# Kernel tuning notes

Hardware: AMD Instinct MI355X
Metric: run time of the kernel (lower is better)

Reference implementation:

```python
import jax, jax.numpy as jnp
import numpy as np

OUT_SIZE = 7      # roi_layer out_size
SAMPLE_NUM = 2    # roi_layer sample_num
STRIDES = (4, 8, 16, 32)
IMG = 1024.0


def _roi_align(feat_nchw, rois, out, scale, sn):
    """mmdet RoIAlign (aligned=False), vectorized over all rois.

    feat_nchw: [B, C, H, W]; rois: [N, 5] = (batch_idx, x1, y1, x2, y2).
    Returns [N, C, out, out].
    """
    feat = jnp.transpose(feat_nchw, (0, 2, 3, 1))  # [B, H, W, C]
    B, H, W, C = feat.shape
    N = rois.shape[0]
    b = rois[:, 0].astype(jnp.int32)
    x1 = rois[:, 1] * scale
    y1 = rois[:, 2] * scale
    x2 = rois[:, 3] * scale
    y2 = rois[:, 4] * scale
    roi_w = jnp.maximum(x2 - x1, 1.0)
    roi_h = jnp.maximum(y2 - y1, 1.0)
    # sample-point offsets within the roi, in bin units: [out*sn]
    grid = (jnp.arange(out, dtype=jnp.float32)[:, None]
            + (jnp.arange(sn, dtype=jnp.float32)[None, :] + 0.5) / sn).reshape(-1)
    ys = y1[:, None] + grid[None, :] * (roi_h / out)[:, None]  # [N, S]
    xs = x1[:, None] + grid[None, :] * (roi_w / out)[:, None]  # [N, S]

    def interp1(coord, size):
        valid = ((coord > -1.0) & (coord < size)).astype(coord.dtype)
        c = jnp.clip(coord, 0.0, size - 1.0)
        lo = jnp.floor(c).astype(jnp.int32)
        hi = jnp.minimum(lo + 1, size - 1)
        w_hi = c - lo.astype(coord.dtype)
        w_lo = 1.0 - w_hi
        # zero-out out-of-image samples via the weights
        return lo, hi, w_lo * valid, w_hi * valid

    y_lo, y_hi, wy_lo, wy_hi = interp1(ys, H)
    x_lo, x_hi, wx_lo, wx_hi = interp1(xs, W)

    def gather(yi, xi):
        # [N, S, S, C]
        return feat[b[:, None, None], yi[:, :, None], xi[:, None, :]]

    val = (gather(y_lo, x_lo) * (wy_lo[:, :, None] * wx_lo[:, None, :])[..., None]
           + gather(y_lo, x_hi) * (wy_lo[:, :, None] * wx_hi[:, None, :])[..., None]
           + gather(y_hi, x_lo) * (wy_hi[:, :, None] * wx_lo[:, None, :])[..., None]
           + gather(y_hi, x_hi) * (wy_hi[:, :, None] * wx_hi[:, None, :])[..., None])
    # average the sn x sn samples inside each bin
    val = val.reshape(N, out, sn, out, sn, C).mean(axis=(2, 4))  # [N, out, out, C]
    return jnp.transpose(val, (0, 3, 1, 2))  # [N, C, out, out]


def setup_inputs() -> dict:
    key = jax.random.key(0)
    ks = jax.random.split(key, 8)
    feats = {}
    for i, hw in enumerate([256, 128, 64, 32]):
        feats[f"feat{i}"] = jax.random.normal(ks[i], (1, 256, hw, hw), dtype=jnp.float32)
    N = 1000
    u = jax.random.uniform(ks[4], (N, 4), dtype=jnp.float32)
    x1 = u[:, 0] * (IMG - 64.0)
    y1 = u[:, 1] * (IMG - 64.0)
    w = 16.0 + u[:, 2] * 480.0
    h = 16.0 + u[:, 3] * 480.0
    x2 = jnp.minimum(x1 + w, IMG - 1.0)
    y2 = jnp.minimum(y1 + h, IMG - 1.0)
    bidx = jnp.zeros((N,), dtype=jnp.float32)
    rois = jnp.stack([bidx, x1, y1, x2, y2], axis=1)
    feats["rois"] = rois
    return feats


def reference(feat0, feat1, feat2, feat3, rois):
    feats = (feat0, feat1, feat2, feat3)
    # PASingleRoIExtractor multi-level path: RoIAlign every roi on every level,
    # then elementwise max across levels.
    out = _roi_align(feats[0], rois, OUT_SIZE, 1.0 / STRIDES[0], SAMPLE_NUM)
    for lvl in range(1, len(feats)):
        out = jnp.maximum(out, _roi_align(feats[lvl], rois, OUT_SIZE,
                                          1.0 / STRIDES[lvl], SAMPLE_NUM))
    return out
```

## Files before the change

kernel.cpp:

```cpp
#include <hip/hip_runtime.h>


#define NCH 256
#define NBIN 49

typedef _Float16 half2v __attribute__((ext_vector_type(2)));

#if defined(__has_builtin)
#if __has_builtin(__builtin_amdgcn_fdot2)
#define HAVE_FDOT2 1
#endif
#if __has_builtin(__builtin_amdgcn_cvt_pkrtz)
#define HAVE_PKRTZ 1
#endif
#endif

__device__ __constant__ int    d_H[4]      = {256, 128, 64, 32};
__device__ __constant__ float  d_scale[4]  = {0.25f, 0.125f, 0.0625f, 0.03125f};
__device__ __constant__ unsigned d_off4b[4] = {0u, 33554432u, 41943040u, 44040192u};
__device__ __constant__ size_t d_offu[4]   = {0, 16777216, 20971520, 22020096};
__device__ __constant__ int    d_P[4]      = {65536, 16384, 4096, 1024};
__device__ __constant__ int    d_t2s[4]    = {0, 2048, 2560, 2688};
__device__ __constant__ int    d_psh[4]    = {9, 7, 5, 3};

__device__ __forceinline__ int pack_h2(float a, float b) {
#ifdef HAVE_PKRTZ
    return __builtin_bit_cast(int, __builtin_amdgcn_cvt_pkrtz(a, b));
#else
    half2v h;
    h.x = (_Float16)a;
    h.y = (_Float16)b;
    return __builtin_bit_cast(int, h);
#endif
}
__device__ __forceinline__ half2v bc_h2(int x) { return __builtin_bit_cast(half2v, x); }
__device__ __forceinline__ half2v bc_h2u(unsigned x) { return __builtin_bit_cast(half2v, x); }

#ifdef HAVE_FDOT2
#define ACC2(uLLc, uLHc, w2, k0)                                                                       \
    acc[k0] = __builtin_amdgcn_fdot2(bc_h2u(__builtin_amdgcn_perm((uLHc), (uLLc), 0x05040100u)), (w2), \
                                     acc[k0], false);                                                  \
    acc[k0 + 1] = __builtin_amdgcn_fdot2(                                                              \
        bc_h2u(__builtin_amdgcn_perm((uLHc), (uLLc), 0x07060302u)), (w2), acc[k0 + 1], false)
#else
#define ACC2(uLLc, uLHc, w2, k0)                                       \
    do {                                                               \
        half2v a_ = bc_h2u(uLLc), b_ = bc_h2u(uLHc);                   \
        float w0_ = (float)(w2).x, w1_ = (float)(w2).y;                \
        acc[k0]     = fmaf((float)a_.x, w0_, acc[k0]);                 \
        acc[k0]     = fmaf((float)b_.x, w1_, acc[k0]);                 \
        acc[k0 + 1] = fmaf((float)a_.y, w0_, acc[k0 + 1]);             \
        acc[k0 + 1] = fmaf((float)b_.y, w1_, acc[k0 + 1]);             \
    } while (0)
#endif

__device__ __forceinline__ void math4(float* acc, const uint4* L, int4 ye, int4 xe) {
    half2v wx = bc_h2(xe.z);
    half2v wlo = bc_h2(ye.z) * wx;
    half2v whi = bc_h2(ye.w) * wx;
    ACC2(L[0].x, L[1].x, wlo, 0);
    ACC2(L[0].y, L[1].y, wlo, 2);
    ACC2(L[0].z, L[1].z, wlo, 4);
    ACC2(L[0].w, L[1].w, wlo, 6);
    ACC2(L[2].x, L[3].x, whi, 0);
    ACC2(L[2].y, L[3].y, whi, 2);
    ACC2(L[2].z, L[3].z, whi, 4);
    ACC2(L[2].w, L[3].w, whi, 6);
}

__device__ __forceinline__ uint4 ldws(const char* __restrict__ wsb, unsigned off) {
    return *(const uint4*)(wsb + off);
}

__global__ __launch_bounds__(256) void transpose_flat(
    const float* __restrict__ f0, const float* __restrict__ f1, const float* __restrict__ f2,
    const float* __restrict__ f3, unsigned short* __restrict__ out) {
    const int b = blockIdx.x;
    const int lvl = (b >= d_t2s[1]) + (b >= d_t2s[2]) + (b >= d_t2s[3]);
    const int rem = b - d_t2s[lvl];
    const int sh = d_psh[lvl];
    const int pb = rem & ((1 << sh) - 1);
    const int cgi = rem >> sh;
    const int P = d_P[lvl];
    const float* in = (lvl == 0) ? f0 : (lvl == 1) ? f1 : (lvl == 2) ? f2 : f3;

    const int tid = threadIdx.x;
    const int o8 = tid & 7;
    const int g = tid >> 3;
    const int p0 = pb * 128 + g * 4;
    const int c0 = cgi * 64 + o8 * 8;

    const float* src = in + (size_t)c0 * P + p0;
    float vv[32];
#pragma unroll
    for (int r = 0; r < 8; ++r)
        *(float4*)&vv[4 * r] = *(const float4*)(src + (size_t)r * P);

    unsigned short* o = out + d_offu[lvl] + (size_t)p0 * NCH + c0;
#pragma unroll
    for (int j = 0; j < 4; ++j) {
        uint4 d;
        d.x = (unsigned)pack_h2(vv[0 * 4 + j], vv[1 * 4 + j]);
        d.y = (unsigned)pack_h2(vv[2 * 4 + j], vv[3 * 4 + j]);
        d.z = (unsigned)pack_h2(vv[4 * 4 + j], vv[5 * 4 + j]);
        d.w = (unsigned)pack_h2(vv[6 * 4 + j], vv[7 * 4 + j]);
        *(uint4*)(o + (size_t)j * NCH) = d;
    }
}

__global__ __launch_bounds__(256, 4) void roi_main4b(const uint4* __restrict__ ws,
                                                     const float* __restrict__ rois,
                                                     float* __restrict__ out) {
    __shared__ float smem[64 * NBIN];
    __shared__ int4 tbl[4][2][14];

    const int n = blockIdx.x >> 2;
    const int quarter = blockIdx.x & 3;
    const int tid = threadIdx.x;
    const float* r = rois + (size_t)n * 5;

    if (tid < 112) {
        int lvl = tid / 28;
        int e = tid % 28;
        int axis = e / 14;
        int s = e % 14;
        int H = d_H[lvl];
        float sc = d_scale[lvl];
        float a = (axis ? r[1] : r[2]) * sc;
        float b2 = (axis ? r[3] : r[4]) * sc;
        float binsz = fmaxf(b2 - a, 1.0f) * (1.0f / 7.0f);
        float g = (float)(s >> 1) + 0.25f + 0.5f * (float)(s & 1);
        float coord = a + g * binsz;
        float valid = (coord > -1.0f && coord < (float)H) ? 1.0f : 0.0f;
        float c = fminf(fmaxf(coord, 0.0f), (float)H - 1.0f);
        int lo = (int)floorf(c);
        int hi = min(lo + 1, H - 1);
        float whi = (c - (float)lo) * valid;
        float wlo = (1.0f - (c - (float)lo)) * valid;
        int mult = axis ? 512 : H * 512;
        int4 t;
        t.x = lo * mult;
        t.y = hi * mult;
        if (axis) {
            t.z = pack_h2(wlo, whi);
            t.w = 0;
        } else {
            t.z = pack_h2(wlo, wlo);
            t.w = pack_h2(whi, whi);
        }
        tbl[lvl][axis][s] = t;
    }
    __syncthreads();

    const int p = tid & 7;
    const int h = tid >> 3;
    const int octet = quarter * 8 + p;
    const char* __restrict__ wsb = (const char*)ws;

    unsigned lvlbase[4];
#pragma unroll
    for (int l = 0; l < 4; ++l) lvlbase[l] = d_off4b[l] + (unsigned)octet * 16u;

#pragma unroll
    for (int pass = 0; pass < 2; ++pass) {
        const int b = h + pass * 32;
        if (b < NBIN) {
            int by = b / 7;
            int bx = b - by * 7;
            float m[8];
#pragma unroll
            for (int k = 0; k < 8; ++k) m[k] = -3.402823e38f;
#pragma unroll
            for (int lvl = 0; lvl < 4; ++lvl) {
                const unsigned base = lvlbase[lvl];
                int4 ye0 = tbl[lvl][0][2 * by];
                int4 ye1 = tbl[lvl][0][2 * by + 1];
                int4 xe0 = tbl[lvl][1][2 * bx];
                int4 xe1 = tbl[lvl][1][2 * bx + 1];
                uint4 L[16];
                L[0]  = ldws(wsb, base + (unsigned)(ye0.x + xe0.x));
                L[1]  = ldws(wsb, base + (unsigned)(ye0.x + xe0.y));
                L[2]  = ldws(wsb, base + (unsigned)(ye0.y + xe0.x));
                L[3]  = ldws(wsb, base + (unsigned)(ye0.y + xe0.y));
                L[4]  = ldws(wsb, base + (unsigned)(ye0.x + xe1.x));
                L[5]  = ldws(wsb, base + (unsigned)(ye0.x + xe1.y));
                L[6]  = ldws(wsb, base + (unsigned)(ye0.y + xe1.x));
                L[7]  = ldws(wsb, base + (unsigned)(ye0.y + xe1.y));
                L[8]  = ldws(wsb, base + (unsigned)(ye1.x + xe0.x));
                L[9]  = ldws(wsb, base + (unsigned)(ye1.x + xe0.y));
                L[10] = ldws(wsb, base + (unsigned)(ye1.y + xe0.x));
                L[11] = ldws(wsb, base + (unsigned)(ye1.y + xe0.y));
                L[12] = ldws(wsb, base + (unsigned)(ye1.x + xe1.x));
                L[13] = ldws(wsb, base + (unsigned)(ye1.x + xe1.y));
                L[14] = ldws(wsb, base + (unsigned)(ye1.y + xe1.x));
                L[15] = ldws(wsb, base + (unsigned)(ye1.y + xe1.y));
                float acc[8];
#pragma unroll
                for (int k = 0; k < 8; ++k) acc[k] = 0.0f;
                math4(acc, &L[0], ye0, xe0);
                math4(acc, &L[4], ye0, xe1);
                math4(acc, &L[8], ye1, xe0);
                math4(acc, &L[12], ye1, xe1);
#pragma unroll
                for (int k = 0; k < 8; ++k) m[k] = fmaxf(m[k], acc[k] * 0.25f);
            }
#pragma unroll
            for (int k = 0; k < 8; ++k) smem[(p * 8 + k) * NBIN + b] = m[k];
        }
    }
    __syncthreads();

    float4* o4 = (float4*)(out + (size_t)n * (NCH * NBIN) + (size_t)quarter * (64 * NBIN));
    const float4* s4 = (const float4*)smem;
    for (int i = tid; i < 64 * NBIN / 4; i += 256) o4[i] = s4[i];
}

__device__ __forceinline__ int4 make_entry_f(float coord, int size, int mult) {
    float valid = (coord > -1.0f && coord < (float)size) ? 1.0f : 0.0f;
    float c = fminf(fmaxf(coord, 0.0f), (float)size - 1.0f);
    int lo = (int)floorf(c);
    int hi = min(lo + 1, size - 1);
    float whi = (c - (float)lo) * valid;
    float wlo = (1.0f - (c - (float)lo)) * valid;
    int4 r;
    r.x = lo * mult;
    r.y = hi * mult;
    r.z = __float_as_int(wlo);
    r.w = __float_as_int(whi);
    return r;
}

__global__ __launch_bounds__(256) void roi_direct(
    const float* __restrict__ f0, const float* __restrict__ f1, const float* __restrict__ f2,
    const float* __restrict__ f3, const float* __restrict__ rois, float* __restrict__ out) {
    const int n = blockIdx.x;
    const int c = threadIdx.x;
    const float* feats[4] = {f0, f1, f2, f3};
    const float* r = rois + (size_t)n * 5;
    for (int b = 0; b < NBIN; ++b) {
        int by = b / 7;
        int bx = b - by * 7;
        float m = -3.402823e38f;
#pragma unroll
        for (int lvl = 0; lvl < 4; ++lvl) {
            int H = d_H[lvl];
            float sc = d_scale[lvl];
            float x1 = r[1] * sc, y1 = r[2] * sc, x2 = r[3] * sc, y2 = r[4] * sc;
            float bw = fmaxf(x2 - x1, 1.0f) * (1.0f / 7.0f);
            float bh = fmaxf(y2 - y1, 1.0f) * (1.0f / 7.0f);
            const float* f = feats[lvl] + (size_t)c * H * H;
            float acc = 0.0f;
#pragma unroll
            for (int sy = 0; sy < 2; ++sy) {
#pragma unroll
                for (int sx = 0; sx < 2; ++sx) {
                    float yc = y1 + ((float)by + 0.25f + 0.5f * sy) * bh;
                    float xc = x1 + ((float)bx + 0.25f + 0.5f * sx) * bw;
                    int4 ey = make_entry_f(yc, H, H);
                    int4 ex = make_entry_f(xc, H, 1);
                    float wyl = __int_as_float(ey.z), wyh = __int_as_float(ey.w);
                    float wxl = __int_as_float(ex.z), wxh = __int_as_float(ex.w);
                    acc += f[ey.x + ex.x] * wyl * wxl + f[ey.x + ex.y] * wyl * wxh +
                           f[ey.y + ex.x] * wyh * wxl + f[ey.y + ex.y] * wyh * wxh;
                }
            }
            m = fmaxf(m, acc * 0.25f);
        }
        out[((size_t)n * NCH + c) * NBIN + b] = m;
    }
}

extern "C" void kernel_launch(void* const* d_in, const int* in_sizes, int n_in, void* d_out,
                              int out_size, void* d_ws, size_t ws_size, hipStream_t stream) {
    const float* f0 = (const float*)d_in[0];
    const float* f1 = (const float*)d_in[1];
    const float* f2 = (const float*)d_in[2];
    const float* f3 = (const float*)d_in[3];
    const float* rois = (const float*)d_in[4];
    const int nrois = in_sizes[4] / 5;
    float* out = (float*)d_out;

    const size_t need = 44564480;
    if (ws_size < need) {
        roi_direct<<<nrois, 256, 0, stream>>>(f0, f1, f2, f3, rois, out);
        return;
    }
    unsigned short* wsp = (unsigned short*)d_ws;
    transpose_flat<<<2720, 256, 0, stream>>>(f0, f1, f2, f3, wsp);
    roi_main4b<<<4 * nrois, 256, 0, stream>>>((const uint4*)d_ws, rois, out);
}
```

Baseline: 204.7 us.

## Double-buffer per-level gathers with sched barriers to overlap loads and math

Restructures the per-bin level loop into a two-buffer software pipeline. The next level's 16 gather loads are issued before the current level's interpolation math runs, and sched_barrier fences keep the compiler from reordering them. Launch bounds drop from 4 to 2 blocks per CU to make room for the extra registers the doubled load buffers need. The aim is to hide gather latency inside each wave, at the cost of fewer resident waves to hide latency across waves.

```diff
diff --git a/kernel.cpp b/kernel.cpp
--- a/kernel.cpp
+++ b/kernel.cpp
@@ -72,6 +72,39 @@
     return *(const uint4*)(wsb + off);
 }
 
+__device__ __forceinline__ void issue16(uint4* L, const char* __restrict__ wsb, unsigned base,
+                                        int4 ye0, int4 ye1, int4 xe0, int4 xe1) {
+    L[0]  = ldws(wsb, base + (unsigned)(ye0.x + xe0.x));
+    L[1]  = ldws(wsb, base + (unsigned)(ye0.x + xe0.y));
+    L[2]  = ldws(wsb, base + (unsigned)(ye0.y + xe0.x));
+    L[3]  = ldws(wsb, base + (unsigned)(ye0.y + xe0.y));
+    L[4]  = ldws(wsb, base + (unsigned)(ye0.x + xe1.x));
+    L[5]  = ldws(wsb, base + (unsigned)(ye0.x + xe1.y));
+    L[6]  = ldws(wsb, base + (unsigned)(ye0.y + xe1.x));
+    L[7]  = ldws(wsb, base + (unsigned)(ye0.y + xe1.y));
+    L[8]  = ldws(wsb, base + (unsigned)(ye1.x + xe0.x));
+    L[9]  = ldws(wsb, base + (unsigned)(ye1.x + xe0.y));
+    L[10] = ldws(wsb, base + (unsigned)(ye1.y + xe0.x));
+    L[11] = ldws(wsb, base + (unsigned)(ye1.y + xe0.y));
+    L[12] = ldws(wsb, base + (unsigned)(ye1.x + xe1.x));
+    L[13] = ldws(wsb, base + (unsigned)(ye1.x + xe1.y));
+    L[14] = ldws(wsb, base + (unsigned)(ye1.y + xe1.x));
+    L[15] = ldws(wsb, base + (unsigned)(ye1.y + xe1.y));
+}
+
+__device__ __forceinline__ void math_stage(float* m, const uint4* L, int4 ye0, int4 ye1,
+                                           int4 xe0, int4 xe1) {
+    float acc[8];
+#pragma unroll
+    for (int k = 0; k < 8; ++k) acc[k] = 0.0f;
+    math4(acc, &L[0], ye0, xe0);
+    math4(acc, &L[4], ye0, xe1);
+    math4(acc, &L[8], ye1, xe0);
+    math4(acc, &L[12], ye1, xe1);
+#pragma unroll
+    for (int k = 0; k < 8; ++k) m[k] = fmaxf(m[k], acc[k] * 0.25f);
+}
+
 __global__ __launch_bounds__(256) void transpose_flat(
     const float* __restrict__ f0, const float* __restrict__ f1, const float* __restrict__ f2,
     const float* __restrict__ f3, unsigned short* __restrict__ out) {
@@ -108,7 +141,7 @@
     }
 }
 
-__global__ __launch_bounds__(256, 4) void roi_main4b(const uint4* __restrict__ ws,
+__global__ __launch_bounds__(256, 2) void roi_main4b(const uint4* __restrict__ ws,
                                                      const float* __restrict__ rois,
                                                      float* __restrict__ out) {
     __shared__ float smem[64 * NBIN];
@@ -161,6 +194,15 @@
 #pragma unroll
     for (int l = 0; l < 4; ++l) lvlbase[l] = d_off4b[l] + (unsigned)octet * 16u;
 
+#define RD_E(E, lvl)                     \
+    E##y0 = tbl[lvl][0][2 * by];         \
+    E##y1 = tbl[lvl][0][2 * by + 1];     \
+    E##x0 = tbl[lvl][1][2 * bx];         \
+    E##x1 = tbl[lvl][1][2 * bx + 1]
+#define ISSUE(L, E, lvl) issue16(L, wsb, lvlbase[lvl], E##y0, E##y1, E##x0, E##x1)
+#define MATH(L, E) math_stage(m, L, E##y0, E##y1, E##x0, E##x1)
+#define FENCE() __builtin_amdgcn_sched_barrier(0)
+
 #pragma unroll
     for (int pass = 0; pass < 2; ++pass) {
         const int b = h + pass * 32;
@@ -170,44 +212,37 @@
             float m[8];
 #pragma unroll
             for (int k = 0; k < 8; ++k) m[k] = -3.402823e38f;
-#pragma unroll
-            for (int lvl = 0; lvl < 4; ++lvl) {
-                const unsigned base = lvlbase[lvl];
-                int4 ye0 = tbl[lvl][0][2 * by];
-                int4 ye1 = tbl[lvl][0][2 * by + 1];
-                int4 xe0 = tbl[lvl][1][2 * bx];
-                int4 xe1 = tbl[lvl][1][2 * bx + 1];
-                uint4 L[16];
-                L[0]  = ldws(wsb, base + (unsigned)(ye0.x + xe0.x));
-                L[1]  = ldws(wsb, base + (unsigned)(ye0.x + xe0.y));
-                L[2]  = ldws(wsb, base + (unsigned)(ye0.y + xe0.x));
-                L[3]  = ldws(wsb, base + (unsigned)(ye0.y + xe0.y));
-                L[4]  = ldws(wsb, base + (unsigned)(ye0.x + xe1.x));
-                L[5]  = ldws(wsb, base + (unsigned)(ye0.x + xe1.y));
-                L[6]  = ldws(wsb, base + (unsigned)(ye0.y + xe1.x));
-                L[7]  = ldws(wsb, base + (unsigned)(ye0.y + xe1.y));
-                L[8]  = ldws(wsb, base + (unsigned)(ye1.x + xe0.x));
-                L[9]  = ldws(wsb, base + (unsigned)(ye1.x + xe0.y));
-                L[10] = ldws(wsb, base + (unsigned)(ye1.y + xe0.x));
-                L[11] = ldws(wsb, base + (unsigned)(ye1.y + xe0.y));
-                L[12] = ldws(wsb, base + (unsigned)(ye1.x + xe1.x));
-                L[13] = ldws(wsb, base + (unsigned)(ye1.x + xe1.y));
-                L[14] = ldws(wsb, base + (unsigned)(ye1.y + xe1.x));
-                L[15] = ldws(wsb, base + (unsigned)(ye1.y + xe1.y));
-                float acc[8];
-#pragma unroll
-                for (int k = 0; k < 8; ++k) acc[k] = 0.0f;
-                math4(acc, &L[0], ye0, xe0);
-                math4(acc, &L[4], ye0, xe1);
-                math4(acc, &L[8], ye1, xe0);
-                math4(acc, &L[12], ye1, xe1);
-#pragma unroll
-                for (int k = 0; k < 8; ++k) m[k] = fmaxf(m[k], acc[k] * 0.25f);
-            }
+
+            uint4 LA[16], LB[16];
+            int4 Ay0, Ay1, Ax0, Ax1, By0, By1, Bx0, Bx1;
+
+            RD_E(A, 0);
+            ISSUE(LA, A, 0);
+            RD_E(B, 1);
+            ISSUE(LB, B, 1);
+            FENCE();
+            MATH(LA, A);
+            FENCE();
+            RD_E(A, 2);
+            ISSUE(LA, A, 2);
+            FENCE();
+            MATH(LB, B);
+            FENCE();
+            RD_E(B, 3);
+            ISSUE(LB, B, 3);
+            FENCE();
+            MATH(LA, A);
+            FENCE();
+            MATH(LB, B);
+
 #pragma unroll
             for (int k = 0; k < 8; ++k) smem[(p * 8 + k) * NBIN + b] = m[k];
         }
     }
+#undef RD_E
+#undef ISSUE
+#undef MATH
+#undef FENCE
     __syncthreads();
 
     float4* o4 = (float4*)(out + (size_t)n * (NCH * NBIN) + (size_t)quarter * (64 * NBIN));
```

Result: no change. 203.9 us (-0.4%).
